# Kernel optimization log

Measured on AMD Instinct MI355X. Metric: run time of the kernel, lower is better.

Reference implementation:

```python
import jax, jax.numpy as jnp
import numpy as np

B = 32768
HID = 512          # hidden_dim
DIM = 256          # output dim
MAX_N = 17         # max_n + 1
KEY_MID = (MAX_N + HID) // 2   # 264
DEC_MID = (HID + DIM) // 2     # 384
SP_MID = (HID + MAX_N) // 2    # 264


def _linear_params(k, fan_in, fan_out):
    k1, k2 = jax.random.split(k)
    lim = 1.0 / np.sqrt(fan_in)
    W = jax.random.uniform(k1, (fan_in, fan_out), minval=-lim, maxval=lim, dtype=jnp.float32)
    b = jax.random.uniform(k2, (fan_out,), minval=-lim, maxval=lim, dtype=jnp.float32)
    return W, b


def setup_inputs() -> dict:
    key = jax.random.key(0)
    ks = jax.random.split(key, 7)
    z = jax.random.normal(ks[0], (B, HID), dtype=jnp.float32)
    key_W1, key_b1 = _linear_params(ks[1], MAX_N, KEY_MID)
    key_W2, key_b2 = _linear_params(ks[2], KEY_MID, HID)
    dec_W1, dec_b1 = _linear_params(ks[3], HID, DEC_MID)
    dec_W2, dec_b2 = _linear_params(ks[4], DEC_MID, DIM)
    sp_W1, sp_b1 = _linear_params(ks[5], HID, SP_MID)
    sp_W2, sp_b2 = _linear_params(ks[6], SP_MID, MAX_N)
    return dict(
        z=z,
        key_W1=key_W1, key_b1=key_b1,
        key_g1=jnp.ones((KEY_MID,), jnp.float32), key_be1=jnp.zeros((KEY_MID,), jnp.float32),
        key_W2=key_W2, key_b2=key_b2,
        dec_W1=dec_W1, dec_b1=dec_b1, dec_W2=dec_W2, dec_b2=dec_b2,
        sp_W1=sp_W1, sp_b1=sp_b1,
        sp_g1=jnp.ones((SP_MID,), jnp.float32), sp_be1=jnp.zeros((SP_MID,), jnp.float32),
        sp_W2=sp_W2, sp_b2=sp_b2,
    )


def _ln(x, g, b):
    m = x.mean(-1, keepdims=True)
    v = x.var(-1, keepdims=True)
    return (x - m) / jnp.sqrt(v + 1e-5) * g + b


def _ragged_indices(n):
    # n: np.int array [B]; returns batch ids and within-sample positions k
    n = np.asarray(n)
    batch = np.repeat(np.arange(n.shape[0]), n)
    starts = np.concatenate([np.zeros(1, dtype=np.int64), np.cumsum(n)[:-1]])
    k = np.arange(batch.shape[0]) - starts[batch]
    return batch, k


def reference(z, key_W1, key_b1, key_g1, key_be1, key_W2, key_b2,
              dec_W1, dec_b1, dec_W2, dec_b2,
              sp_W1, sp_b1, sp_g1, sp_be1, sp_W2, sp_b2):
    # size_pred MLP: Linear -> LayerNorm -> ReLU -> Linear
    h = jax.nn.relu(_ln(z @ sp_W1 + sp_b1, sp_g1, sp_be1))
    n_pred = h @ sp_W2 + sp_b2                       # [B, MAX_N]
    n = np.asarray(jnp.argmax(n_pred, axis=-1))      # concrete sizes (ragged)
    batch_np, k_np = _ragged_indices(n)
    batch = jnp.asarray(batch_np)
    k = jnp.asarray(k_np)
    pos = jax.nn.one_hot(k, MAX_N, dtype=jnp.float32)            # [T, MAX_N]
    # key_net: Linear -> LayerNorm -> ReLU -> Linear
    keys = jax.nn.relu(_ln(pos @ key_W1 + key_b1, key_g1, key_be1)) @ key_W2 + key_b2  # [T, HID]
    vals_rep = z[batch]                              # repeat_interleave via gather
    zp = vals_rep * keys
    # decoder: Linear -> ReLU -> Linear (no layernorm by default)
    x = jax.nn.relu(zp @ dec_W1 + dec_b1) @ dec_W2 + dec_b2      # [T, DIM]
    return x, batch
```

## Files before the change

### kernel.cpp

```cpp
#include <hip/hip_runtime.h>
#include <hip/hip_bf16.h>

#define B_N   32768
#define HID   512
#define DIM   256
#define MAXN  17
#define SM    264
#define DM    384

typedef __attribute__((ext_vector_type(8))) short bf16x8;
typedef __attribute__((ext_vector_type(4))) float f32x4;

#define AS1 __attribute__((address_space(1)))
#define AS3 __attribute__((address_space(3)))

static __device__ __forceinline__ unsigned short f2bf(float x) {
  union { float f; unsigned u; } v; v.f = x;
  unsigned r = (v.u + 0x7FFFu + ((v.u >> 16) & 1u)) >> 16;
  return (unsigned short)r;
}

static __device__ __forceinline__ unsigned pkbf(float a, float b) {
  __hip_bfloat162 h = __float22bfloat162_rn(float2{a, b});
  union { __hip_bfloat162 h; unsigned u; } cv; cv.h = h;
  return cv.u;
}

__global__ __launch_bounds__(320, 3) void sizepred_kernel(
    const float* __restrict__ z,  const float* __restrict__ W1,
    const float* __restrict__ b1, const float* __restrict__ g1,
    const float* __restrict__ be1, const float* __restrict__ W2,
    const float* __restrict__ b2, int* __restrict__ n_out)
{
  __shared__ __align__(16) char smem[33024 + 2 * 8448];
  float* zs  = (float*)smem;
  float* us  = (float*)smem;
  float* wb0 = (float*)(smem + 33024);
  float* wb1 = (float*)(smem + 33024 + 8448);
  __shared__ float lnm[16], lnr[16];
  __shared__ float log17[16 * 17];

  const int tid = threadIdx.x;
  const int b0  = blockIdx.x * 16;
  const int wv  = tid >> 6;
  const int ln  = tid & 63;

  const bool act = tid < 264;
  const int  s0  = (tid / 66) * 4;
  const int  j0  = (tid % 66) * 4;

  float acc[4][4];
#pragma unroll
  for (int i = 0; i < 4; ++i)
#pragma unroll
    for (int q = 0; q < 4; ++q) acc[i][q] = 0.f;

  for (int s = wv; s < 32; s += 5) {
    int r = s >> 1, sl = s & 1;
    const float* gp = z + (size_t)(b0 + r) * 512 + sl * 256 + ln * 4;
    __builtin_amdgcn_global_load_lds(
        (const AS1 unsigned*)gp,
        (AS3 unsigned*)(zs + r * 516 + sl * 256), 16, 0, 0);
  }
  {
    const float* gc = W1;
    const float* gp1 = gc + (size_t)(wv * 64 + ln) * 4;
    __builtin_amdgcn_global_load_lds(
        (const AS1 unsigned*)gp1, (AS3 unsigned*)(wb0 + wv * 256), 16, 0, 0);
    if (wv < 3) {
      const float* gp2 = gc + (size_t)((wv + 5) * 64 + ln) * 4;
      __builtin_amdgcn_global_load_lds(
          (const AS1 unsigned*)gp2, (AS3 unsigned*)(wb0 + (wv + 5) * 256), 16, 0, 0);
    } else if (wv == 3) {
      const float* gp2 = gc + 2048 + ln;
      __builtin_amdgcn_global_load_lds(
          (const AS1 unsigned*)gp2, (AS3 unsigned*)(wb0 + 2048), 4, 0, 0);
    }
  }
  __syncthreads();

  float* cw = wb0;
  float* nw = wb1;
#pragma unroll 1
  for (int ch = 0; ch < 64; ++ch) {
    if (ch + 1 < 64) {
      const float* gc = W1 + (size_t)(ch + 1) * 2112;
      const float* gp1 = gc + (size_t)(wv * 64 + ln) * 4;
      __builtin_amdgcn_global_load_lds(
          (const AS1 unsigned*)gp1, (AS3 unsigned*)(nw + wv * 256), 16, 0, 0);
      if (wv < 3) {
        const float* gp2 = gc + (size_t)((wv + 5) * 64 + ln) * 4;
        __builtin_amdgcn_global_load_lds(
            (const AS1 unsigned*)gp2, (AS3 unsigned*)(nw + (wv + 5) * 256), 16, 0, 0);
      } else if (wv == 3) {
        const float* gp2 = gc + 2048 + ln;
        __builtin_amdgcn_global_load_lds(
            (const AS1 unsigned*)gp2, (AS3 unsigned*)(nw + 2048), 4, 0, 0);
      }
    }
    if (act) {
      const int zb = ch * 8;
#pragma unroll
      for (int u = 0; u < 2; ++u) {
        float4 za0 = *(const float4*)&zs[(s0 + 0) * 516 + zb + u * 4];
        float4 za1 = *(const float4*)&zs[(s0 + 1) * 516 + zb + u * 4];
        float4 za2 = *(const float4*)&zs[(s0 + 2) * 516 + zb + u * 4];
        float4 za3 = *(const float4*)&zs[(s0 + 3) * 516 + zb + u * 4];
#pragma unroll
        for (int e = 0; e < 4; ++e) {
          float4 w = *(const float4*)&cw[(u * 4 + e) * 264 + j0];
          float a0 = (e == 0) ? za0.x : (e == 1) ? za0.y : (e == 2) ? za0.z : za0.w;
          float a1 = (e == 0) ? za1.x : (e == 1) ? za1.y : (e == 2) ? za1.z : za1.w;
          float a2 = (e == 0) ? za2.x : (e == 1) ? za2.y : (e == 2) ? za2.z : za2.w;
          float a3 = (e == 0) ? za3.x : (e == 1) ? za3.y : (e == 2) ? za3.z : za3.w;
          acc[0][0] += a0 * w.x; acc[0][1] += a0 * w.y; acc[0][2] += a0 * w.z; acc[0][3] += a0 * w.w;
          acc[1][0] += a1 * w.x; acc[1][1] += a1 * w.y; acc[1][2] += a1 * w.z; acc[1][3] += a1 * w.w;
          acc[2][0] += a2 * w.x; acc[2][1] += a2 * w.y; acc[2][2] += a2 * w.z; acc[2][3] += a2 * w.w;
          acc[3][0] += a3 * w.x; acc[3][1] += a3 * w.y; acc[3][2] += a3 * w.z; acc[3][3] += a3 * w.w;
        }
      }
    }
    float* t = cw; cw = nw; nw = t;
    __syncthreads();
  }

  float4 o0, o1, o2, o3;
  if (act) {
    float4 bb = *(const float4*)&b1[j0];
    o0.x = acc[0][0] + bb.x; o0.y = acc[0][1] + bb.y; o0.z = acc[0][2] + bb.z; o0.w = acc[0][3] + bb.w;
    o1.x = acc[1][0] + bb.x; o1.y = acc[1][1] + bb.y; o1.z = acc[1][2] + bb.z; o1.w = acc[1][3] + bb.w;
    o2.x = acc[2][0] + bb.x; o2.y = acc[2][1] + bb.y; o2.z = acc[2][2] + bb.z; o2.w = acc[2][3] + bb.w;
    o3.x = acc[3][0] + bb.x; o3.y = acc[3][1] + bb.y; o3.z = acc[3][2] + bb.z; o3.w = acc[3][3] + bb.w;
  }
  __syncthreads();
  if (act) {
    *(float4*)&us[(s0 + 0) * 268 + j0] = o0;
    *(float4*)&us[(s0 + 1) * 268 + j0] = o1;
    *(float4*)&us[(s0 + 2) * 268 + j0] = o2;
    *(float4*)&us[(s0 + 3) * 268 + j0] = o3;
  }
  __syncthreads();

  if (tid < 16) {
    float s = 0.f, q = 0.f;
    for (int j = 0; j < 264; ++j) { float v = us[tid * 268 + j]; s += v; q += v * v; }
    float m   = s / 264.f;
    float var = q / 264.f - m * m;
    lnm[tid] = m;
    lnr[tid] = 1.f / sqrtf(var + 1e-5f);
  }
  __syncthreads();

  for (int idx = tid; idx < 16 * 264; idx += 320) {
    int s = idx / 264, j = idx - s * 264;
    float v = (us[s * 268 + j] - lnm[s]) * lnr[s] * g1[j] + be1[j];
    us[s * 268 + j] = fmaxf(v, 0.f);
  }
  __syncthreads();

  if (tid < 272) {
    int s = tid / 17, jj = tid - s * 17;
    float a = b2[jj];
    const float* up = &us[s * 268];
#pragma unroll 4
    for (int c = 0; c < 264; c += 4) {
      float4 u = *(const float4*)(up + c);
      a += u.x * W2[(c + 0) * 17 + jj];
      a += u.y * W2[(c + 1) * 17 + jj];
      a += u.z * W2[(c + 2) * 17 + jj];
      a += u.w * W2[(c + 3) * 17 + jj];
    }
    log17[tid] = a;
  }
  __syncthreads();

  if (tid < 16) {
    int best = 0; float bv = log17[tid * 17];
    for (int jj = 1; jj < 17; ++jj) {
      float v = log17[tid * 17 + jj];
      if (v > bv) { bv = v; best = jj; }
    }
    n_out[b0 + tid] = best;
  }
}

__global__ __launch_bounds__(1024) void scan_kernel(const int* __restrict__ n,
                                                    int* __restrict__ starts)
{
  __shared__ int part[1024];
  const int tid  = threadIdx.x;
  const int base = tid * 32;
  int loc[32];
  int s = 0;
#pragma unroll
  for (int i = 0; i < 8; ++i) {
    int4 v = ((const int4*)(n + base))[i];
    loc[i * 4 + 0] = v.x; loc[i * 4 + 1] = v.y;
    loc[i * 4 + 2] = v.z; loc[i * 4 + 3] = v.w;
    s += v.x + v.y + v.z + v.w;
  }
  part[tid] = s;
  __syncthreads();
  for (int off = 1; off < 1024; off <<= 1) {
    int v   = part[tid];
    int add = (tid >= off) ? part[tid - off] : 0;
    __syncthreads();
    part[tid] = v + add;
    __syncthreads();
  }
  int run = part[tid] - s;
#pragma unroll
  for (int i = 0; i < 8; ++i) {
    int4 w;
    w.x = run; run += loc[i * 4 + 0];
    w.y = run; run += loc[i * 4 + 1];
    w.z = run; run += loc[i * 4 + 2];
    w.w = run; run += loc[i * 4 + 3];
    ((int4*)(starts + base))[i] = w;
  }
  if (tid == 1023) starts[B_N] = run;
}

__global__ __launch_bounds__(256) void scatter_kernel(
    const int* __restrict__ n, const int* __restrict__ starts,
    int* __restrict__ bi, int* __restrict__ ki, float* __restrict__ out, int T)
{
  int b = blockIdx.x * 256 + threadIdx.x;
  if (b >= B_N) return;
  int st = starts[b], nn = n[b];
  float* ob = out + (size_t)T * DIM;
  for (int k = 0; k < nn; ++k) {
    bi[st + k] = b;
    ki[st + k] = k;
    ob[st + k] = (float)b;
  }
}

__global__ __launch_bounds__(320) void keys_kernel(
    const float* __restrict__ W1, const float* __restrict__ b1,
    const float* __restrict__ g1, const float* __restrict__ be1,
    const float* __restrict__ W2, const float* __restrict__ b2,
    float* __restrict__ ktab)
{
  __shared__ float hs[264];
  __shared__ float mr[2];
  const int kk = blockIdx.x, tid = threadIdx.x;
  if (tid < 264) hs[tid] = W1[kk * 264 + tid] + b1[tid];
  __syncthreads();
  if (tid == 0) {
    float s = 0.f, q = 0.f;
    for (int j = 0; j < 264; ++j) { float v = hs[j]; s += v; q += v * v; }
    float m = s / 264.f;
    mr[0] = m;
    mr[1] = 1.f / sqrtf(q / 264.f - m * m + 1e-5f);
  }
  __syncthreads();
  if (tid < 264) hs[tid] = fmaxf((hs[tid] - mr[0]) * mr[1] * g1[tid] + be1[tid], 0.f);
  __syncthreads();
  for (int c = tid; c < 512; c += 320) {
    float a = b2[c];
    for (int j = 0; j < 264; ++j) a += hs[j] * W2[j * 512 + c];
    ktab[kk * 512 + c] = a;
  }
}

__global__ __launch_bounds__(64) void pack_kernel(
    const float* __restrict__ W1, const float* __restrict__ W2,
    short* __restrict__ W1p, short* __restrict__ W2p)
{
  const int g = blockIdx.x, l = threadIdx.x;
  const float* W; int nt, kt, N;
  if (g < 384) { W = W1; kt = g / 24; nt = g % 24; N = 384; }
  else         { W = W2; int gg = g - 384; kt = gg / 16; nt = gg % 16; N = 256; }
  const int krow = kt * 32 + ((l >> 4) << 3);
  const int col  = nt * 16 + (l & 15);
  short v[8];
#pragma unroll
  for (int j = 0; j < 8; ++j)
    v[j] = (short)f2bf(W[(size_t)(krow + j) * N + col]);
  short* d = (g < 384) ? (W1p + ((size_t)g * 64 + l) * 8)
                       : (W2p + ((size_t)(g - 384) * 64 + l) * 8);
  *(bf16x8*)d = *(bf16x8*)v;
}

__global__ __launch_bounds__(256, 4) void decoder_kernel(
    const float* __restrict__ z,  const float* __restrict__ ktab,
    const short* __restrict__ W1p, const float* __restrict__ b1,
    const short* __restrict__ W2p, const float* __restrict__ b2,
    const int* __restrict__ bi,   const int* __restrict__ ki,
    float* __restrict__ out, int T)
{
  __shared__ __align__(16) short zps[16384];
  __shared__ int tb[32], tk[32];

  const int tid  = threadIdx.x;
  const int wave = tid >> 6;
  const int lane = tid & 63;
  const int t0   = blockIdx.x * 32;

  if (tid < 32) {
    int t = t0 + tid;
    tb[tid] = (t < T) ? bi[t] : 0;
    tk[tid] = (t < T) ? ki[t] : 0;
  }
  __syncthreads();

#pragma unroll
  for (int it = 0; it < 8; ++it) {
    int chunk = tid + it * 256;
    int l  = chunk & 63;
    int mt = (chunk >> 6) & 1;
    int kt = chunk >> 7;
    int m  = mt * 16 + (l & 15);
    int k0 = kt * 32 + ((l >> 4) << 3);
    const float4* zr = (const float4*)(z    + (size_t)tb[m] * 512 + k0);
    const float4* kr = (const float4*)(ktab + (size_t)tk[m] * 512 + k0);
    float4 z0 = zr[0], z1 = zr[1], k4 = kr[0], k5 = kr[1];
    uint4 u;
    u.x = pkbf(z0.x * k4.x, z0.y * k4.y);
    u.y = pkbf(z0.z * k4.z, z0.w * k4.w);
    u.z = pkbf(z1.x * k5.x, z1.y * k5.y);
    u.w = pkbf(z1.z * k5.z, z1.w * k5.w);
    *(uint4*)&zps[(size_t)chunk * 8] = u;
  }
  __syncthreads();

  f32x4 acc[2][6];
#pragma unroll
  for (int mt = 0; mt < 2; ++mt)
#pragma unroll
    for (int j = 0; j < 6; ++j) acc[mt][j] = (f32x4){0.f, 0.f, 0.f, 0.f};

  {
    const short* wb = W1p + ((size_t)(wave * 6) * 64 + lane) * 8;
#pragma unroll 4
    for (int kt = 0; kt < 16; ++kt) {
      bf16x8 a0 = *(bf16x8*)&zps[((kt * 2 + 0) * 64 + lane) * 8];
      bf16x8 a1 = *(bf16x8*)&zps[((kt * 2 + 1) * 64 + lane) * 8];
#pragma unroll
      for (int j = 0; j < 6; ++j) {
        bf16x8 bf = *(const bf16x8*)(wb + (size_t)kt * 12288 + j * 512);
        acc[0][j] = __builtin_amdgcn_mfma_f32_16x16x32_bf16(a0, bf, acc[0][j], 0, 0, 0);
        acc[1][j] = __builtin_amdgcn_mfma_f32_16x16x32_bf16(a1, bf, acc[1][j], 0, 0, 0);
      }
    }
  }
  __syncthreads();

  {
    short* Hs = zps;
    float bload[6];
#pragma unroll
    for (int j = 0; j < 6; ++j)
      bload[j] = b1[wave * 96 + j * 16 + (lane & 15)];
#pragma unroll
    for (int mt = 0; mt < 2; ++mt) {
#pragma unroll
      for (int j = 0; j < 6; ++j) {
        int c = wave * 96 + j * 16 + (lane & 15);
        int lane2hi = ((c >> 3) & 3) << 4;
        int koff = (c >> 5) * 2;
        int jj = c & 7;
        int mbase = mt * 16 + (lane >> 4) * 4;
        int a0 = ((koff + (mbase >> 4)) * 64 + ((mbase & 15) | lane2hi)) * 8 + jj;
        float v0 = fmaxf(acc[mt][j][0] + bload[j], 0.f);
        float v1 = fmaxf(acc[mt][j][1] + bload[j], 0.f);
        float v2 = fmaxf(acc[mt][j][2] + bload[j], 0.f);
        float v3 = fmaxf(acc[mt][j][3] + bload[j], 0.f);
        unsigned p01 = pkbf(v0, v1);
        unsigned p23 = pkbf(v2, v3);
        Hs[a0 +  0] = (short)(p01 & 0xFFFFu);
        Hs[a0 +  8] = (short)(p01 >> 16);
        Hs[a0 + 16] = (short)(p23 & 0xFFFFu);
        Hs[a0 + 24] = (short)(p23 >> 16);
      }
    }
  }
  __syncthreads();

  f32x4 acc2[2][4];
#pragma unroll
  for (int mt = 0; mt < 2; ++mt)
#pragma unroll
    for (int j = 0; j < 4; ++j) acc2[mt][j] = (f32x4){0.f, 0.f, 0.f, 0.f};

  {
    const short* Hs = zps;
    const short* wb = W2p + ((size_t)(wave * 4) * 64 + lane) * 8;
#pragma unroll 4
    for (int kt = 0; kt < 12; ++kt) {
      bf16x8 a0 = *(const bf16x8*)&Hs[((kt * 2 + 0) * 64 + lane) * 8];
      bf16x8 a1 = *(const bf16x8*)&Hs[((kt * 2 + 1) * 64 + lane) * 8];
#pragma unroll
      for (int j = 0; j < 4; ++j) {
        bf16x8 bf = *(const bf16x8*)(wb + (size_t)kt * 8192 + j * 512);
        acc2[0][j] = __builtin_amdgcn_mfma_f32_16x16x32_bf16(a0, bf, acc2[0][j], 0, 0, 0);
        acc2[1][j] = __builtin_amdgcn_mfma_f32_16x16x32_bf16(a1, bf, acc2[1][j], 0, 0, 0);
      }
    }
  }

  {
    float bload[4];
#pragma unroll
    for (int j = 0; j < 4; ++j)
      bload[j] = b2[wave * 64 + j * 16 + (lane & 15)];
#pragma unroll
    for (int mt = 0; mt < 2; ++mt) {
#pragma unroll
      for (int r = 0; r < 4; ++r) {
        int t = t0 + mt * 16 + (lane >> 4) * 4 + r;
        if (t < T) {
#pragma unroll
          for (int j = 0; j < 4; ++j) {
            int c = wave * 64 + j * 16 + (lane & 15);
            out[(size_t)t * 256 + c] = acc2[mt][j][r] + bload[j];
          }
        }
      }
    }
  }
}

extern "C" void kernel_launch(void* const* d_in, const int* in_sizes, int n_in,
                              void* d_out, int out_size, void* d_ws, size_t ws_size,
                              hipStream_t stream)
{
  const float* z      = (const float*)d_in[0];
  const float* keyW1  = (const float*)d_in[1];
  const float* keyb1  = (const float*)d_in[2];
  const float* keyg1  = (const float*)d_in[3];
  const float* keybe1 = (const float*)d_in[4];
  const float* keyW2  = (const float*)d_in[5];
  const float* keyb2  = (const float*)d_in[6];
  const float* decW1  = (const float*)d_in[7];
  const float* decb1  = (const float*)d_in[8];
  const float* decW2  = (const float*)d_in[9];
  const float* decb2  = (const float*)d_in[10];
  const float* spW1   = (const float*)d_in[11];
  const float* spb1   = (const float*)d_in[12];
  const float* spg1   = (const float*)d_in[13];
  const float* spbe1  = (const float*)d_in[14];
  const float* spW2   = (const float*)d_in[15];
  const float* spb2   = (const float*)d_in[16];

  const int T = out_size / (DIM + 1);

  char* ws = (char*)d_ws;
  int*   n_arr  = (int*)(ws);
  int*   starts = (int*)(ws + 131072);
  float* ktab   = (float*)(ws + 262160);
  short* W1p    = (short*)(ws + 296976);
  short* W2p    = (short*)(ws + 690192);
  int*   bi     = (int*)(ws + 886800);
  size_t kioff  = 886800 + (((size_t)T * 4 + 15) / 16) * 16;
  int*   ki     = (int*)(ws + kioff);

  float* outF = (float*)d_out;

  sizepred_kernel<<<B_N / 16, 320, 0, stream>>>(z, spW1, spb1, spg1, spbe1, spW2, spb2, n_arr);
  pack_kernel<<<576, 64, 0, stream>>>(decW1, decW2, W1p, W2p);
  scan_kernel<<<1, 1024, 0, stream>>>(n_arr, starts);
  keys_kernel<<<MAXN, 320, 0, stream>>>(keyW1, keyb1, keyg1, keybe1, keyW2, keyb2, ktab);
  scatter_kernel<<<B_N / 256, 256, 0, stream>>>(n_arr, starts, bi, ki, outF, T);
  if (T > 0)
    decoder_kernel<<<(T + 31) / 32, 256, 0, stream>>>(z, ktab, W1p, decb1, W2p, decb2, bi, ki, outF, T);
}
```

Baseline: 1.127 ms.

## Double decoder row tile to 64 tokens with 8 waves in a 2x4 grid

The decoder block now handles 64 tokens with 512 threads arranged as 2 row groups by 4 column groups. Each weight fragment loaded from global memory is reused across twice as many rows, halving weight traffic per token. LDS use doubles to 64KB per block, and the 512-thread, 4-blocks launch bound tightens register limits, which may lower occupancy or cause spills.

```diff
diff --git a/kernel.cpp b/kernel.cpp
--- a/kernel.cpp
+++ b/kernel.cpp
@@ -283,22 +283,24 @@
   *(bf16x8*)d = *(bf16x8*)v;
 }
 
-__global__ __launch_bounds__(256, 4) void decoder_kernel(
+__global__ __launch_bounds__(512, 4) void decoder_kernel(
     const float* __restrict__ z,  const float* __restrict__ ktab,
     const short* __restrict__ W1p, const float* __restrict__ b1,
     const short* __restrict__ W2p, const float* __restrict__ b2,
     const int* __restrict__ bi,   const int* __restrict__ ki,
     float* __restrict__ out, int T)
 {
-  __shared__ __align__(16) short zps[16384];
-  __shared__ int tb[32], tk[32];
+  __shared__ __align__(16) short zps[32768];
+  __shared__ int tb[64], tk[64];
 
   const int tid  = threadIdx.x;
   const int wave = tid >> 6;
   const int lane = tid & 63;
-  const int t0   = blockIdx.x * 32;
-
-  if (tid < 32) {
+  const int wr   = wave >> 2;
+  const int wc   = wave & 3;
+  const int t0   = blockIdx.x * 64;
+
+  if (tid < 64) {
     int t = t0 + tid;
     tb[tid] = (t < T) ? bi[t] : 0;
     tk[tid] = (t < T) ? ki[t] : 0;
@@ -307,12 +309,12 @@
 
 #pragma unroll
   for (int it = 0; it < 8; ++it) {
-    int chunk = tid + it * 256;
-    int l  = chunk & 63;
-    int mt = (chunk >> 6) & 1;
-    int kt = chunk >> 7;
-    int m  = mt * 16 + (l & 15);
-    int k0 = kt * 32 + ((l >> 4) << 3);
+    int chunk = tid + it * 512;
+    int l   = chunk & 63;
+    int mtg = (chunk >> 6) & 3;
+    int kt  = chunk >> 8;
+    int m   = mtg * 16 + (l & 15);
+    int k0  = kt * 32 + ((l >> 4) << 3);
     const float4* zr = (const float4*)(z    + (size_t)tb[m] * 512 + k0);
     const float4* kr = (const float4*)(ktab + (size_t)tk[m] * 512 + k0);
     float4 z0 = zr[0], z1 = zr[1], k4 = kr[0], k5 = kr[1];
@@ -332,11 +334,11 @@
     for (int j = 0; j < 6; ++j) acc[mt][j] = (f32x4){0.f, 0.f, 0.f, 0.f};
 
   {
-    const short* wb = W1p + ((size_t)(wave * 6) * 64 + lane) * 8;
+    const short* wb = W1p + ((size_t)(wc * 6) * 64 + lane) * 8;
 #pragma unroll 4
     for (int kt = 0; kt < 16; ++kt) {
-      bf16x8 a0 = *(bf16x8*)&zps[((kt * 2 + 0) * 64 + lane) * 8];
-      bf16x8 a1 = *(bf16x8*)&zps[((kt * 2 + 1) * 64 + lane) * 8];
+      bf16x8 a0 = *(bf16x8*)&zps[((kt * 4 + wr * 2 + 0) * 64 + lane) * 8];
+      bf16x8 a1 = *(bf16x8*)&zps[((kt * 4 + wr * 2 + 1) * 64 + lane) * 8];
 #pragma unroll
       for (int j = 0; j < 6; ++j) {
         bf16x8 bf = *(const bf16x8*)(wb + (size_t)kt * 12288 + j * 512);
@@ -352,17 +354,17 @@
     float bload[6];
 #pragma unroll
     for (int j = 0; j < 6; ++j)
-      bload[j] = b1[wave * 96 + j * 16 + (lane & 15)];
+      bload[j] = b1[wc * 96 + j * 16 + (lane & 15)];
 #pragma unroll
     for (int mt = 0; mt < 2; ++mt) {
 #pragma unroll
       for (int j = 0; j < 6; ++j) {
-        int c = wave * 96 + j * 16 + (lane & 15);
+        int c = wc * 96 + j * 16 + (lane & 15);
         int lane2hi = ((c >> 3) & 3) << 4;
-        int koff = (c >> 5) * 2;
+        int ktp = (c >> 5) * 4;
         int jj = c & 7;
-        int mbase = mt * 16 + (lane >> 4) * 4;
-        int a0 = ((koff + (mbase >> 4)) * 64 + ((mbase & 15) | lane2hi)) * 8 + jj;
+        int mbase = wr * 32 + mt * 16 + (lane >> 4) * 4;
+        int a0 = ((ktp + (mbase >> 4)) * 64 + ((mbase & 15) | lane2hi)) * 8 + jj;
         float v0 = fmaxf(acc[mt][j][0] + bload[j], 0.f);
         float v1 = fmaxf(acc[mt][j][1] + bload[j], 0.f);
         float v2 = fmaxf(acc[mt][j][2] + bload[j], 0.f);
@@ -386,11 +388,11 @@
 
   {
     const short* Hs = zps;
-    const short* wb = W2p + ((size_t)(wave * 4) * 64 + lane) * 8;
+    const short* wb = W2p + ((size_t)(wc * 4) * 64 + lane) * 8;
 #pragma unroll 4
     for (int kt = 0; kt < 12; ++kt) {
-      bf16x8 a0 = *(const bf16x8*)&Hs[((kt * 2 + 0) * 64 + lane) * 8];
-      bf16x8 a1 = *(const bf16x8*)&Hs[((kt * 2 + 1) * 64 + lane) * 8];
+      bf16x8 a0 = *(const bf16x8*)&Hs[((kt * 4 + wr * 2 + 0) * 64 + lane) * 8];
+      bf16x8 a1 = *(const bf16x8*)&Hs[((kt * 4 + wr * 2 + 1) * 64 + lane) * 8];
 #pragma unroll
       for (int j = 0; j < 4; ++j) {
         bf16x8 bf = *(const bf16x8*)(wb + (size_t)kt * 8192 + j * 512);
@@ -404,16 +406,16 @@
     float bload[4];
 #pragma unroll
     for (int j = 0; j < 4; ++j)
-      bload[j] = b2[wave * 64 + j * 16 + (lane & 15)];
+      bload[j] = b2[wc * 64 + j * 16 + (lane & 15)];
 #pragma unroll
     for (int mt = 0; mt < 2; ++mt) {
 #pragma unroll
       for (int r = 0; r < 4; ++r) {
-        int t = t0 + mt * 16 + (lane >> 4) * 4 + r;
+        int t = t0 + wr * 32 + mt * 16 + (lane >> 4) * 4 + r;
         if (t < T) {
 #pragma unroll
           for (int j = 0; j < 4; ++j) {
-            int c = wave * 64 + j * 16 + (lane & 15);
+            int c = wc * 64 + j * 16 + (lane & 15);
             out[(size_t)t * 256 + c] = acc2[mt][j][r] + bload[j];
           }
         }
@@ -464,5 +466,5 @@
   keys_kernel<<<MAXN, 320, 0, stream>>>(keyW1, keyb1, keyg1, keybe1, keyW2, keyb2, ktab);
   scatter_kernel<<<B_N / 256, 256, 0, stream>>>(n_arr, starts, bi, ki, outF, T);
   if (T > 0)
-    decoder_kernel<<<(T + 31) / 32, 256, 0, stream>>>(z, ktab, W1p, decb1, W2p, decb2, bi, ki, outF, T);
-}
+    decoder_kernel<<<(T + 63) / 64, 512, 0, stream>>>(z, ktab, W1p, decb1, W2p, decb2, bi, ki, outF, T);
+}
```

New measurement: 1.163 ms. 3.2% more time.
